# Kernel optimization log

Hardware: AMD Instinct MI355X
Metric: run time of the kernel (lower is better)

Reference implementation:

```python
import jax, jax.numpy as jnp
import numpy as np

N, F, P, O, E = 20000, 8, 12, 32, 320000


def setup_inputs() -> dict:
    key = jax.random.key(0)
    ks = jax.random.split(key, 18)
    g = lambda k, shape: (jax.random.normal(k, shape, jnp.float32) * 0.1)
    x = jax.random.normal(ks[0], (N, F, P), jnp.float32)
    edge_index = jax.random.randint(ks[1], (2, E), 0, N, dtype=jnp.int32)
    return {
        "x": x,
        "edge_index": edge_index,
        # GCNConv weights/biases for update (z), reset (r), candidate (h) gates
        "Wz": g(ks[2], (F, O)), "bz": g(ks[3], (O,)),
        "Wr": g(ks[4], (F, O)), "br": g(ks[5], (O,)),
        "Wh": g(ks[6], (F, O)), "bh": g(ks[7], (O,)),
        # GRU linear layers (torch.nn.Linear: y = x @ W.T + b), in=2*O, out=O
        "lz_w": g(ks[8], (O, 2 * O)), "lz_b": g(ks[9], (O,)),
        "lr_w": g(ks[10], (O, 2 * O)), "lr_b": g(ks[11], (O,)),
        "lh_w": g(ks[12], (O, 2 * O)), "lh_b": g(ks[13], (O,)),
        # temporal attention logits over periods
        "att": g(ks[14], (P,)),
        # final Linear(32 -> window_size)
        "out_w": g(ks[15], (P, O)), "out_b": g(ks[16], (P,)),
    }


def reference(x, edge_index, Wz, bz, Wr, br, Wh, bh,
              lz_w, lz_b, lr_w, lr_b, lh_w, lh_b, att, out_w, out_b):
    n = x.shape[0]
    # gcn_norm with self-loops: norm_e = d^-1/2[src] * d^-1/2[dst]
    loop = jnp.arange(n, dtype=edge_index.dtype)
    src = jnp.concatenate([edge_index[0], loop])
    dst = jnp.concatenate([edge_index[1], loop])
    deg = jax.ops.segment_sum(jnp.ones(src.shape[0], x.dtype), dst, num_segments=n)
    dinv = jnp.where(deg > 0, deg ** -0.5, 0.0)
    norm = dinv[src] * dinv[dst]  # [E+n]

    def gcn(xp, W, b):
        # xp: [n, P, F] -> [n, P, O]; GCNConv: D^-1/2 (A+I) D^-1/2 (X W) + b
        h = jnp.einsum('npf,fo->npo', xp, W)
        msg = h[src] * norm[:, None, None]  # [E+n, P, O]
        return jax.ops.segment_sum(msg, dst, num_segments=n) + b

    xp = jnp.transpose(x, (0, 2, 1))  # [n, P, F]
    # A3TGCN does NOT carry H across periods (H stays initial zeros), so all
    # periods are independent GRU steps from H = 0 and can be batched.
    H = jnp.zeros(xp.shape[:2] + (O,), x.dtype)
    Z = jax.nn.sigmoid(jnp.concatenate([gcn(xp, Wz, bz), H], -1) @ lz_w.T + lz_b)
    R = jax.nn.sigmoid(jnp.concatenate([gcn(xp, Wr, br), H], -1) @ lr_w.T + lr_b)
    Ht = jnp.tanh(jnp.concatenate([gcn(xp, Wh, bh), H * R], -1) @ lh_w.T + lh_b)
    Hp = Z * H + (1.0 - Z) * Ht  # [n, P, O]
    probs = jax.nn.softmax(att)
    Hacc = jnp.einsum('npo,p->no', Hp, probs)  # attention-weighted sum
    return jax.nn.relu(Hacc) @ out_w.T + out_b  # [n, window_size]
```

## Files before the change

### kernel.cpp

```cpp
#include <hip/hip_runtime.h>
#include <math.h>

#define FP 96
#define SLOT 64
#define NPB 8
#define GBLK 128
#define PBLK 256

__device__ __forceinline__ unsigned f2bf_bits(float f) {
    unsigned u = __float_as_uint(f);
    return (u + 0x7fffu + ((u >> 16) & 1u)) >> 16;
}
__device__ __forceinline__ float bf_lo(unsigned u) { return __uint_as_float(u << 16); }
__device__ __forceinline__ float bf_hi(unsigned u) { return __uint_as_float(u & 0xffff0000u); }

__global__ void k_pre(const float* __restrict__ Wz, const float* __restrict__ bz,
                      const float* __restrict__ Wh, const float* __restrict__ bh,
                      const float* __restrict__ lz_w, const float* __restrict__ lz_b,
                      const float* __restrict__ lh_w, const float* __restrict__ lh_b,
                      const float* __restrict__ att, const float* __restrict__ out_w,
                      const float* __restrict__ out_b, const float* __restrict__ x,
                      float* __restrict__ cst, int* __restrict__ cnt,
                      unsigned* __restrict__ xb, int N) {
    int b = blockIdx.x, t = threadIdx.x;
    if (b == 0) {
        int f = t >> 5, o = t & 31;
        float sz = 0.f, sh = 0.f;
        for (int j = 0; j < 32; ++j) {
            sz += Wz[f * 32 + j] * lz_w[o * 64 + j];
            sh += Wh[f * 32 + j] * lh_w[o * 64 + j];
        }
        cst[t]       = sz;
        cst[256 + t] = sh;
        if (t < 32) {
            float a = lz_b[t], c = lh_b[t];
            for (int j = 0; j < 32; ++j) {
                a += bz[j] * lz_w[t * 64 + j];
                c += bh[j] * lh_w[t * 64 + j];
            }
            cst[512 + t] = a;
            cst[544 + t] = c;
        }
        if (t < 12) {
            float m = -1e30f;
            for (int p = 0; p < 12; ++p) m = fmaxf(m, att[p]);
            float s = 0.f;
            for (int p = 0; p < 12; ++p) s += expf(att[p] - m);
            cst[576 + t] = expf(att[t] - m) / s;
        }
        for (int i = t; i < 384; i += PBLK)
            cst[588 + (i & 31) * 12 + (i >> 5)] = out_w[i];
        if (t < 12) cst[972 + t] = out_b[t];
    } else {
        int i = (b - 1) * PBLK + t;
        if (i < N * 12) {
            int n = i / 12;
            if (i - n * 12 == 0) cnt[n] = 0;
            const float4* x4 = (const float4*)x;
            float4 a = x4[i * 2], c = x4[i * 2 + 1];
            uint4 r;
            r.x = f2bf_bits(a.x) | (f2bf_bits(a.y) << 16);
            r.y = f2bf_bits(a.z) | (f2bf_bits(a.w) << 16);
            r.z = f2bf_bits(c.x) | (f2bf_bits(c.y) << 16);
            r.w = f2bf_bits(c.z) | (f2bf_bits(c.w) << 16);
            ((uint4*)xb)[i] = r;
        }
    }
}

__global__ void k_histfill(const int* __restrict__ ei, int E,
                           int* __restrict__ cnt, int* __restrict__ bucket) {
    int e = blockIdx.x * blockDim.x + threadIdx.x;
    if (e >= E) return;
    int src = ei[e], dst = ei[E + e];
    int pos = atomicAdd(cnt + dst, 1);
    if (pos < SLOT) bucket[(size_t)dst * SLOT + pos] = src;
}

__global__ void __launch_bounds__(GBLK)
k_gather_gates(const unsigned* __restrict__ xb, const int* __restrict__ cnt,
               const int* __restrict__ bucket, const float* __restrict__ cst,
               float* __restrict__ out, int N) {
    __shared__ float sy[NPB][FP + 4];
    __shared__ float shr[NPB][32];
    __shared__ float scst[984];
    __shared__ int   sbuck[NPB][68];
    __shared__ int   sdeg[NPB];
    int t = threadIdx.x;
    for (int i = t; i < 984; i += GBLK) scst[i] = cst[i];

    int n0 = blockIdx.x * NPB;
    if (t < NPB) sdeg[t] = (n0 + t < N) ? cnt[n0 + t] : 0;
    {
        int nd = t >> 4, q = t & 15, n = n0 + nd;
        if (n < N) *(int4*)&sbuck[nd][q * 4] =
            ((const int4*)(bucket + (size_t)n * SLOT))[q];
    }
    __syncthreads();

    const uint4* xrow = (const uint4*)xb;
    if (t < NPB * 12) {
        int nl = t / 12, k = t - nl * 12, n = n0 + nl;
        if (n < N) {
            int c = sdeg[nl];
            int deg = min(c, SLOT);
            float di = rsqrtf((float)(c + 1));
            uint4 v = xrow[n * 12 + k];
            float acc[8] = {di * bf_lo(v.x), di * bf_hi(v.x), di * bf_lo(v.y), di * bf_hi(v.y),
                            di * bf_lo(v.z), di * bf_hi(v.z), di * bf_lo(v.w), di * bf_hi(v.w)};
            int j = 0;
            for (; j + 4 <= deg; j += 4) {
                int s0 = sbuck[nl][j],     s1 = sbuck[nl][j + 1];
                int s2 = sbuck[nl][j + 2], s3 = sbuck[nl][j + 3];
                uint4 v0 = xrow[s0 * 12 + k], v1 = xrow[s1 * 12 + k];
                uint4 v2 = xrow[s2 * 12 + k], v3 = xrow[s3 * 12 + k];
                float w0 = rsqrtf((float)(cnt[s0] + 1));
                float w1 = rsqrtf((float)(cnt[s1] + 1));
                float w2 = rsqrtf((float)(cnt[s2] + 1));
                float w3 = rsqrtf((float)(cnt[s3] + 1));
                acc[0] = fmaf(w0, bf_lo(v0.x), fmaf(w1, bf_lo(v1.x), fmaf(w2, bf_lo(v2.x), fmaf(w3, bf_lo(v3.x), acc[0]))));
                acc[1] = fmaf(w0, bf_hi(v0.x), fmaf(w1, bf_hi(v1.x), fmaf(w2, bf_hi(v2.x), fmaf(w3, bf_hi(v3.x), acc[1]))));
                acc[2] = fmaf(w0, bf_lo(v0.y), fmaf(w1, bf_lo(v1.y), fmaf(w2, bf_lo(v2.y), fmaf(w3, bf_lo(v3.y), acc[2]))));
                acc[3] = fmaf(w0, bf_hi(v0.y), fmaf(w1, bf_hi(v1.y), fmaf(w2, bf_hi(v2.y), fmaf(w3, bf_hi(v3.y), acc[3]))));
                acc[4] = fmaf(w0, bf_lo(v0.z), fmaf(w1, bf_lo(v1.z), fmaf(w2, bf_lo(v2.z), fmaf(w3, bf_lo(v3.z), acc[4]))));
                acc[5] = fmaf(w0, bf_hi(v0.z), fmaf(w1, bf_hi(v1.z), fmaf(w2, bf_hi(v2.z), fmaf(w3, bf_hi(v3.z), acc[5]))));
                acc[6] = fmaf(w0, bf_lo(v0.w), fmaf(w1, bf_lo(v1.w), fmaf(w2, bf_lo(v2.w), fmaf(w3, bf_lo(v3.w), acc[6]))));
                acc[7] = fmaf(w0, bf_hi(v0.w), fmaf(w1, bf_hi(v1.w), fmaf(w2, bf_hi(v2.w), fmaf(w3, bf_hi(v3.w), acc[7]))));
            }
            for (; j < deg; ++j) {
                int s = sbuck[nl][j];
                uint4 w4 = xrow[s * 12 + k];
                float w = rsqrtf((float)(cnt[s] + 1));
                acc[0] = fmaf(w, bf_lo(w4.x), acc[0]); acc[1] = fmaf(w, bf_hi(w4.x), acc[1]);
                acc[2] = fmaf(w, bf_lo(w4.y), acc[2]); acc[3] = fmaf(w, bf_hi(w4.y), acc[3]);
                acc[4] = fmaf(w, bf_lo(w4.z), acc[4]); acc[5] = fmaf(w, bf_hi(w4.z), acc[5]);
                acc[6] = fmaf(w, bf_lo(w4.w), acc[6]); acc[7] = fmaf(w, bf_hi(w4.w), acc[7]);
            }
#pragma unroll
            for (int i = 0; i < 8; ++i) sy[nl][k * 8 + i] = di * acc[i];
        }
    }
    __syncthreads();

    int o = t & 31;
#pragma unroll
    for (int it = 0; it < 2; ++it) {
        int local = (t >> 5) + it * 4, n = n0 + local;
        if (n < N) {
            float cz = scst[512 + o], ch = scst[544 + o];
            float hacc = 0.f;
#pragma unroll
            for (int p = 0; p < 12; ++p) {
                float az = cz, ah = ch;
#pragma unroll
                for (int f = 0; f < 8; ++f) {
                    float xf = sy[local][f * 12 + p];
                    az += xf * scst[f * 32 + o];
                    ah += xf * scst[256 + f * 32 + o];
                }
                float Z  = 1.f / (1.f + expf(-az));
                float Ht = tanhf(ah);
                hacc += scst[576 + p] * (1.f - Z) * Ht;
            }
            shr[local][o] = fmaxf(hacc, 0.f);
        }
    }
    __syncthreads();
#pragma unroll
    for (int it = 0; it < 2; ++it) {
        int local = (t >> 5) + it * 4, n = n0 + local;
        if (n < N && o < 12) {
            float s = scst[972 + o];
#pragma unroll
            for (int j2 = 0; j2 < 32; ++j2)
                s += shr[local][j2] * scst[588 + j2 * 12 + o];
            out[(size_t)n * 12 + o] = s;
        }
    }
}

extern "C" void kernel_launch(void* const* d_in, const int* in_sizes, int n_in,
                              void* d_out, int out_size, void* d_ws, size_t ws_size,
                              hipStream_t stream) {
    const float* x    = (const float*)d_in[0];
    const int*   ei   = (const int*)d_in[1];
    const float* Wz   = (const float*)d_in[2];
    const float* bz   = (const float*)d_in[3];
    const float* Wh   = (const float*)d_in[6];
    const float* bh   = (const float*)d_in[7];
    const float* lz_w = (const float*)d_in[8];
    const float* lz_b = (const float*)d_in[9];
    const float* lh_w = (const float*)d_in[12];
    const float* lh_b = (const float*)d_in[13];
    const float* att  = (const float*)d_in[14];
    const float* ow   = (const float*)d_in[15];
    const float* ob   = (const float*)d_in[16];
    float* out = (float*)d_out;

    int N = in_sizes[0] / FP;
    int E = in_sizes[1] / 2;

    int*      cnt    = (int*)d_ws;
    int*      bucket = cnt + N;
    unsigned* xb     = (unsigned*)(bucket + (size_t)N * SLOT);
    float*    cst    = (float*)(xb + (size_t)N * 48);

    int CB = (N * 12 + PBLK - 1) / PBLK;
    k_pre     <<<1 + CB, PBLK, 0, stream>>>(Wz, bz, Wh, bh, lz_w, lz_b, lh_w, lh_b,
                                            att, ow, ob, x, cst, cnt, xb, N);
    k_histfill<<<(E + 255) / 256, 256, 0, stream>>>(ei, E, cnt, bucket);
    k_gather_gates<<<(N + NPB - 1) / NPB, GBLK, 0, stream>>>(xb, cnt, bucket, cst, out, N);
}
```

Before: 145.1 us.

## Prescale bf16 features by source degree norm and pad neighbor lists with zero row

Moves the bf16 conversion of x into a separate kernel that runs after the degree histogram, so each node's features are stored already multiplied by its own d^-1/2. This removes the per-edge random load of cnt[src] and the rsqrt from the gather loop, which becomes plain adds. Neighbor lists are padded to multiples of 8 with an index pointing at an appended all-zero row, so the loop unrolls by 8 with no remainder. The cost is an extra kernel launch and an extra write and read of the bf16 feature buffer, plus one more rounding step because the scaling is applied before bf16 conversion.

Result: no change. 143.4 us (-1.1%).

```diff
diff --git a/kernel.cpp b/kernel.cpp
--- a/kernel.cpp
+++ b/kernel.cpp
@@ -14,58 +14,46 @@
 __device__ __forceinline__ float bf_lo(unsigned u) { return __uint_as_float(u << 16); }
 __device__ __forceinline__ float bf_hi(unsigned u) { return __uint_as_float(u & 0xffff0000u); }
 
-__global__ void k_pre(const float* __restrict__ Wz, const float* __restrict__ bz,
-                      const float* __restrict__ Wh, const float* __restrict__ bh,
-                      const float* __restrict__ lz_w, const float* __restrict__ lz_b,
-                      const float* __restrict__ lh_w, const float* __restrict__ lh_b,
-                      const float* __restrict__ att, const float* __restrict__ out_w,
-                      const float* __restrict__ out_b, const float* __restrict__ x,
-                      float* __restrict__ cst, int* __restrict__ cnt,
-                      unsigned* __restrict__ xb, int N) {
+__global__ void k_zero_fold(int* __restrict__ cnt, int N,
+                            const float* __restrict__ Wz, const float* __restrict__ bz,
+                            const float* __restrict__ Wh, const float* __restrict__ bh,
+                            const float* __restrict__ lz_w, const float* __restrict__ lz_b,
+                            const float* __restrict__ lh_w, const float* __restrict__ lh_b,
+                            const float* __restrict__ att, const float* __restrict__ out_w,
+                            const float* __restrict__ out_b, float* __restrict__ cst) {
     int b = blockIdx.x, t = threadIdx.x;
-    if (b == 0) {
-        int f = t >> 5, o = t & 31;
-        float sz = 0.f, sh = 0.f;
+    if (b < gridDim.x - 1) {
+        int i = b * PBLK + t;
+        if (i < N) cnt[i] = 0;
+        return;
+    }
+    int f = t >> 5, o = t & 31;
+    float sz = 0.f, sh = 0.f;
+    for (int j = 0; j < 32; ++j) {
+        sz += Wz[f * 32 + j] * lz_w[o * 64 + j];
+        sh += Wh[f * 32 + j] * lh_w[o * 64 + j];
+    }
+    cst[t]       = sz;
+    cst[256 + t] = sh;
+    if (t < 32) {
+        float a = lz_b[t], c = lh_b[t];
         for (int j = 0; j < 32; ++j) {
-            sz += Wz[f * 32 + j] * lz_w[o * 64 + j];
-            sh += Wh[f * 32 + j] * lh_w[o * 64 + j];
-        }
-        cst[t]       = sz;
-        cst[256 + t] = sh;
-        if (t < 32) {
-            float a = lz_b[t], c = lh_b[t];
-            for (int j = 0; j < 32; ++j) {
-                a += bz[j] * lz_w[t * 64 + j];
-                c += bh[j] * lh_w[t * 64 + j];
-            }
-            cst[512 + t] = a;
-            cst[544 + t] = c;
-        }
-        if (t < 12) {
-            float m = -1e30f;
-            for (int p = 0; p < 12; ++p) m = fmaxf(m, att[p]);
-            float s = 0.f;
-            for (int p = 0; p < 12; ++p) s += expf(att[p] - m);
-            cst[576 + t] = expf(att[t] - m) / s;
-        }
-        for (int i = t; i < 384; i += PBLK)
-            cst[588 + (i & 31) * 12 + (i >> 5)] = out_w[i];
-        if (t < 12) cst[972 + t] = out_b[t];
-    } else {
-        int i = (b - 1) * PBLK + t;
-        if (i < N * 12) {
-            int n = i / 12;
-            if (i - n * 12 == 0) cnt[n] = 0;
-            const float4* x4 = (const float4*)x;
-            float4 a = x4[i * 2], c = x4[i * 2 + 1];
-            uint4 r;
-            r.x = f2bf_bits(a.x) | (f2bf_bits(a.y) << 16);
-            r.y = f2bf_bits(a.z) | (f2bf_bits(a.w) << 16);
-            r.z = f2bf_bits(c.x) | (f2bf_bits(c.y) << 16);
-            r.w = f2bf_bits(c.z) | (f2bf_bits(c.w) << 16);
-            ((uint4*)xb)[i] = r;
-        }
-    }
+            a += bz[j] * lz_w[t * 64 + j];
+            c += bh[j] * lh_w[t * 64 + j];
+        }
+        cst[512 + t] = a;
+        cst[544 + t] = c;
+    }
+    if (t < 12) {
+        float m = -1e30f;
+        for (int p = 0; p < 12; ++p) m = fmaxf(m, att[p]);
+        float s = 0.f;
+        for (int p = 0; p < 12; ++p) s += expf(att[p] - m);
+        cst[576 + t] = expf(att[t] - m) / s;
+    }
+    for (int i = t; i < 384; i += PBLK)
+        cst[588 + (i & 31) * 12 + (i >> 5)] = out_w[i];
+    if (t < 12) cst[972 + t] = out_b[t];
 }
 
 __global__ void k_histfill(const int* __restrict__ ei, int E,
@@ -75,6 +63,26 @@
     int src = ei[e], dst = ei[E + e];
     int pos = atomicAdd(cnt + dst, 1);
     if (pos < SLOT) bucket[(size_t)dst * SLOT + pos] = src;
+}
+
+__global__ void k_convert(const float* __restrict__ x, const int* __restrict__ cnt,
+                          unsigned* __restrict__ xb, int N) {
+    int i = blockIdx.x * blockDim.x + threadIdx.x;
+    if (i >= (N + 1) * 12) return;
+    int n = i / 12;
+    if (n == N) {
+        ((uint4*)xb)[i] = make_uint4(0u, 0u, 0u, 0u);
+        return;
+    }
+    float w = rsqrtf((float)(cnt[n] + 1));
+    const float4* x4 = (const float4*)x;
+    float4 a = x4[i * 2], c = x4[i * 2 + 1];
+    uint4 r;
+    r.x = f2bf_bits(w * a.x) | (f2bf_bits(w * a.y) << 16);
+    r.y = f2bf_bits(w * a.z) | (f2bf_bits(w * a.w) << 16);
+    r.z = f2bf_bits(w * c.x) | (f2bf_bits(w * c.y) << 16);
+    r.w = f2bf_bits(w * c.z) | (f2bf_bits(w * c.w) << 16);
+    ((uint4*)xb)[i] = r;
 }
 
 __global__ void __launch_bounds__(GBLK)
@@ -97,45 +105,50 @@
             ((const int4*)(bucket + (size_t)n * SLOT))[q];
     }
     __syncthreads();
+    if (t < NPB * 8) {
+        int nl = t >> 3, q = t & 7;
+        int d = min(sdeg[nl], SLOT);
+        int pos = d + q;
+        if (pos < ((d + 7) & ~7)) sbuck[nl][pos] = N;
+    }
+    __syncthreads();
 
     const uint4* xrow = (const uint4*)xb;
     if (t < NPB * 12) {
         int nl = t / 12, k = t - nl * 12, n = n0 + nl;
         if (n < N) {
             int c = sdeg[nl];
-            int deg = min(c, SLOT);
-            float di = rsqrtf((float)(c + 1));
+            int degp = (min(c, SLOT) + 7) & ~7;
             uint4 v = xrow[n * 12 + k];
-            float acc[8] = {di * bf_lo(v.x), di * bf_hi(v.x), di * bf_lo(v.y), di * bf_hi(v.y),
-                            di * bf_lo(v.z), di * bf_hi(v.z), di * bf_lo(v.w), di * bf_hi(v.w)};
-            int j = 0;
-            for (; j + 4 <= deg; j += 4) {
+            float acc[8] = {bf_lo(v.x), bf_hi(v.x), bf_lo(v.y), bf_hi(v.y),
+                            bf_lo(v.z), bf_hi(v.z), bf_lo(v.w), bf_hi(v.w)};
+            for (int j = 0; j < degp; j += 8) {
                 int s0 = sbuck[nl][j],     s1 = sbuck[nl][j + 1];
                 int s2 = sbuck[nl][j + 2], s3 = sbuck[nl][j + 3];
+                int s4 = sbuck[nl][j + 4], s5 = sbuck[nl][j + 5];
+                int s6 = sbuck[nl][j + 6], s7 = sbuck[nl][j + 7];
                 uint4 v0 = xrow[s0 * 12 + k], v1 = xrow[s1 * 12 + k];
                 uint4 v2 = xrow[s2 * 12 + k], v3 = xrow[s3 * 12 + k];
-                float w0 = rsqrtf((float)(cnt[s0] + 1));
-                float w1 = rsqrtf((float)(cnt[s1] + 1));
-                float w2 = rsqrtf((float)(cnt[s2] + 1));
-                float w3 = rsqrtf((float)(cnt[s3] + 1));
-                acc[0] = fmaf(w0, bf_lo(v0.x), fmaf(w1, bf_lo(v1.x), fmaf(w2, bf_lo(v2.x), fmaf(w3, bf_lo(v3.x), acc[0]))));
-                acc[1] = fmaf(w0, bf_hi(v0.x), fmaf(w1, bf_hi(v1.x), fmaf(w2, bf_hi(v2.x), fmaf(w3, bf_hi(v3.x), acc[1]))));
-                acc[2] = fmaf(w0, bf_lo(v0.y), fmaf(w1, bf_lo(v1.y), fmaf(w2, bf_lo(v2.y), fmaf(w3, bf_lo(v3.y), acc[2]))));
-                acc[3] = fmaf(w0, bf_hi(v0.y), fmaf(w1, bf_hi(v1.y), fmaf(w2, bf_hi(v2.y), fmaf(w3, bf_hi(v3.y), acc[3]))));
-                acc[4] = fmaf(w0, bf_lo(v0.z), fmaf(w1, bf_lo(v1.z), fmaf(w2, bf_lo(v2.z), fmaf(w3, bf_lo(v3.z), acc[4]))));
-                acc[5] = fmaf(w0, bf_hi(v0.z), fmaf(w1, bf_hi(v1.z), fmaf(w2, bf_hi(v2.z), fmaf(w3, bf_hi(v3.z), acc[5]))));
-                acc[6] = fmaf(w0, bf_lo(v0.w), fmaf(w1, bf_lo(v1.w), fmaf(w2, bf_lo(v2.w), fmaf(w3, bf_lo(v3.w), acc[6]))));
-                acc[7] = fmaf(w0, bf_hi(v0.w), fmaf(w1, bf_hi(v1.w), fmaf(w2, bf_hi(v2.w), fmaf(w3, bf_hi(v3.w), acc[7]))));
+                uint4 v4 = xrow[s4 * 12 + k], v5 = xrow[s5 * 12 + k];
+                uint4 v6 = xrow[s6 * 12 + k], v7 = xrow[s7 * 12 + k];
+                acc[0] += ((bf_lo(v0.x) + bf_lo(v1.x)) + (bf_lo(v2.x) + bf_lo(v3.x)))
+                        + ((bf_lo(v4.x) + bf_lo(v5.x)) + (bf_lo(v6.x) + bf_lo(v7.x)));
+                acc[1] += ((bf_hi(v0.x) + bf_hi(v1.x)) + (bf_hi(v2.x) + bf_hi(v3.x)))
+                        + ((bf_hi(v4.x) + bf_hi(v5.x)) + (bf_hi(v6.x) + bf_hi(v7.x)));
+                acc[2] += ((bf_lo(v0.y) + bf_lo(v1.y)) + (bf_lo(v2.y) + bf_lo(v3.y)))
+                        + ((bf_lo(v4.y) + bf_lo(v5.y)) + (bf_lo(v6.y) + bf_lo(v7.y)));
+                acc[3] += ((bf_hi(v0.y) + bf_hi(v1.y)) + (bf_hi(v2.y) + bf_hi(v3.y)))
+                        + ((bf_hi(v4.y) + bf_hi(v5.y)) + (bf_hi(v6.y) + bf_hi(v7.y)));
+                acc[4] += ((bf_lo(v0.z) + bf_lo(v1.z)) + (bf_lo(v2.z) + bf_lo(v3.z)))
+                        + ((bf_lo(v4.z) + bf_lo(v5.z)) + (bf_lo(v6.z) + bf_lo(v7.z)));
+                acc[5] += ((bf_hi(v0.z) + bf_hi(v1.z)) + (bf_hi(v2.z) + bf_hi(v3.z)))
+                        + ((bf_hi(v4.z) + bf_hi(v5.z)) + (bf_hi(v6.z) + bf_hi(v7.z)));
+                acc[6] += ((bf_lo(v0.w) + bf_lo(v1.w)) + (bf_lo(v2.w) + bf_lo(v3.w)))
+                        + ((bf_lo(v4.w) + bf_lo(v5.w)) + (bf_lo(v6.w) + bf_lo(v7.w)));
+                acc[7] += ((bf_hi(v0.w) + bf_hi(v1.w)) + (bf_hi(v2.w) + bf_hi(v3.w)))
+                        + ((bf_hi(v4.w) + bf_hi(v5.w)) + (bf_hi(v6.w) + bf_hi(v7.w)));
             }
-            for (; j < deg; ++j) {
-                int s = sbuck[nl][j];
-                uint4 w4 = xrow[s * 12 + k];
-                float w = rsqrtf((float)(cnt[s] + 1));
-                acc[0] = fmaf(w, bf_lo(w4.x), acc[0]); acc[1] = fmaf(w, bf_hi(w4.x), acc[1]);
-                acc[2] = fmaf(w, bf_lo(w4.y), acc[2]); acc[3] = fmaf(w, bf_hi(w4.y), acc[3]);
-                acc[4] = fmaf(w, bf_lo(w4.z), acc[4]); acc[5] = fmaf(w, bf_hi(w4.z), acc[5]);
-                acc[6] = fmaf(w, bf_lo(w4.w), acc[6]); acc[7] = fmaf(w, bf_hi(w4.w), acc[7]);
-            }
+            float di = rsqrtf((float)(c + 1));
 #pragma unroll
             for (int i = 0; i < 8; ++i) sy[nl][k * 8 + i] = di * acc[i];
         }
@@ -203,11 +216,12 @@
     int*      cnt    = (int*)d_ws;
     int*      bucket = cnt + N;
     unsigned* xb     = (unsigned*)(bucket + (size_t)N * SLOT);
-    float*    cst    = (float*)(xb + (size_t)N * 48);
-
-    int CB = (N * 12 + PBLK - 1) / PBLK;
-    k_pre     <<<1 + CB, PBLK, 0, stream>>>(Wz, bz, Wh, bh, lz_w, lz_b, lh_w, lh_b,
-                                            att, ow, ob, x, cst, cnt, xb, N);
-    k_histfill<<<(E + 255) / 256, 256, 0, stream>>>(ei, E, cnt, bucket);
+    float*    cst    = (float*)(xb + (size_t)(N + 1) * 48);
+
+    int ZB = (N + PBLK - 1) / PBLK;
+    k_zero_fold<<<ZB + 1, PBLK, 0, stream>>>(cnt, N, Wz, bz, Wh, bh, lz_w, lz_b,
+                                             lh_w, lh_b, att, ow, ob, cst);
+    k_histfill <<<(E + 255) / 256, 256, 0, stream>>>(ei, E, cnt, bucket);
+    k_convert  <<<((N + 1) * 12 + PBLK - 1) / PBLK, PBLK, 0, stream>>>(x, cnt, xb, N);
     k_gather_gates<<<(N + NPB - 1) / NPB, GBLK, 0, stream>>>(xb, cnt, bucket, cst, out, N);
 }
```
